# Optimization experiments

Hardware: AMD Instinct MI355X
Metric: run time of the kernel (lower is better)

## Reference

```python
import jax, jax.numpy as jnp
import numpy as np

STRIDE = (1, 1)
PAD = (1, 1)
DIL = (1, 1)
GROUPS = 1
DG = 1  # deformable_groups
KH, KW = 3, 3


def setup_inputs() -> dict:
    key = jax.random.key(0)
    k1, k2, k3, k4 = jax.random.split(key, 4)
    x = jax.random.normal(k1, (8, 256, 64, 64), jnp.float32)
    offset = jax.random.normal(k2, (8, DG * 2 * KH * KW, 64, 64), jnp.float32)
    weight = jax.random.normal(k3, (256, 256, KH, KW), jnp.float32) * 0.05
    bias = jax.random.normal(k4, (256,), jnp.float32)
    return {"x": x, "offset": offset, "weight": weight, "bias": bias}


def _deform_conv2d(x, offset, weight, bias):
    N, C, H, W = x.shape
    Cout = weight.shape[0]
    Ho = (H + 2 * PAD[0] - (DIL[0] * (KH - 1) + 1)) // STRIDE[0] + 1
    Wo = (W + 2 * PAD[1] - (DIL[1] * (KW - 1) + 1)) // STRIDE[1] + 1
    K = KH * KW
    Cg = C // DG

    # offset layout: [N, DG, K, 2(y,x), Ho, Wo]
    off = offset.reshape(N, DG, K, 2, Ho, Wo)

    ky, kx = jnp.meshgrid(jnp.arange(KH), jnp.arange(KW), indexing="ij")
    ky = (ky.reshape(K) * DIL[0]).astype(jnp.float32)  # [K]
    kx = (kx.reshape(K) * DIL[1]).astype(jnp.float32)
    base_y = (jnp.arange(Ho) * STRIDE[0] - PAD[0]).astype(jnp.float32)  # [Ho]
    base_x = (jnp.arange(Wo) * STRIDE[1] - PAD[1]).astype(jnp.float32)  # [Wo]

    # sampling positions [N, DG, K, Ho, Wo]
    py = base_y[None, None, None, :, None] + ky[None, None, :, None, None] + off[:, :, :, 0]
    px = base_x[None, None, None, None, :] + kx[None, None, :, None, None] + off[:, :, :, 1]

    y0f = jnp.floor(py)
    x0f = jnp.floor(px)
    ly = py - y0f
    lx = px - x0f
    hy = 1.0 - ly
    hx = 1.0 - lx
    y0 = y0f.astype(jnp.int32)
    x0 = x0f.astype(jnp.int32)
    y1 = y0 + 1
    x1 = x0 + 1

    img = x.reshape(N, DG, Cg, H * W)

    def gather(yi, xi):
        valid = ((yi >= 0) & (yi < H) & (xi >= 0) & (xi < W)).astype(x.dtype)
        idx = jnp.clip(yi, 0, H - 1) * W + jnp.clip(xi, 0, W - 1)  # [N,DG,K,Ho,Wo]
        flat = idx.reshape(N, DG, 1, K * Ho * Wo)
        v = jnp.take_along_axis(img, flat, axis=3).reshape(N, DG, Cg, K, Ho, Wo)
        return v * valid[:, :, None]

    # bilinear combine -> columns [N, DG, Cg, K, Ho, Wo]
    cols = (
        (hy * hx)[:, :, None] * gather(y0, x0)
        + (hy * lx)[:, :, None] * gather(y0, x1)
        + (ly * hx)[:, :, None] * gather(y1, x0)
        + (ly * lx)[:, :, None] * gather(y1, x1)
    )

    # grouped conv accumulation
    P = Ho * Wo
    cols = cols.reshape(N, GROUPS, C // GROUPS, K, P)
    w = weight.reshape(GROUPS, Cout // GROUPS, C // GROUPS, K)
    out = jnp.einsum("ngckp,gock->ngop", cols, w).reshape(N, Cout, Ho, Wo)
    return out + bias[None, :, None, None]


def reference(x, offset, weight, bias):
    return _deform_conv2d(x, offset, weight, bias)
```

## Files before the change

### kernel.cpp

```cpp
#include <hip/hip_runtime.h>


#define H 64
#define W 64
#define CIN 256
#define COUT 256
#define NIMG 8
#define KTAPS 9
#define CK (CIN * KTAPS)
#define NITER 36

typedef _Float16 f16;
typedef __attribute__((ext_vector_type(4))) _Float16 f16x4;
typedef __attribute__((ext_vector_type(8))) _Float16 f16x8;
typedef __attribute__((ext_vector_type(4))) float f32x4;

__global__ __launch_bounds__(256) void dcn_prep(const float* __restrict__ x,
                                                const float* __restrict__ w,
                                                f16* __restrict__ xt,
                                                f16* __restrict__ wt) {
    const int b = blockIdx.x;
    const int t = threadIdx.x;
    if (b < 512) {
        const int n = b >> 6, pb = b & 63;
        const int q = t & 63;
        const int hg = t >> 6;
        const float* xn = x + (size_t)n * CIN * (H * W) + pb * 64;
        float4 ld[4][4];
#pragma unroll
        for (int j = 0; j < 4; ++j)
#pragma unroll
            for (int pq = 0; pq < 4; ++pq)
                ld[j][pq] = *(const float4*)(xn + (size_t)(q * 4 + j) * (H * W) +
                                             hg * 16 + pq * 4);
        f16* xtn = xt + (size_t)n * (H * W) * CIN + (size_t)(pb * 64 + hg * 16) * CIN + q * 4;
#pragma unroll
        for (int pq = 0; pq < 4; ++pq) {
#pragma unroll
            for (int pe = 0; pe < 4; ++pe) {
                const float* l0 = (const float*)&ld[0][pq];
                const float* l1 = (const float*)&ld[1][pq];
                const float* l2 = (const float*)&ld[2][pq];
                const float* l3 = (const float*)&ld[3][pq];
                f16x4 o = {(f16)l0[pe], (f16)l1[pe], (f16)l2[pe], (f16)l3[pe]};
                *(f16x4*)(xtn + (size_t)(pq * 4 + pe) * CIN) = o;
            }
        }
    } else {
        __shared__ f16 tw[CK];
        const int co = b - 512;
        const float* wr = w + (size_t)co * CK + t * 9;
        float v[9];
#pragma unroll
        for (int j = 0; j < 9; ++j) v[j] = wr[j];
#pragma unroll
        for (int j = 0; j < 9; ++j) tw[j * 256 + t] = (f16)v[j];
        __syncthreads();
        f16* o = wt + (size_t)co * CK;
        for (int i = t; i < CK / 8; i += 256)
            *(f16x8*)(o + i * 8) = *(const f16x8*)(tw + i * 8);
    }
}

__global__ __launch_bounds__(256, 2) void dcn_mfma(
    const f16* __restrict__ xt, const float* __restrict__ offset,
    const f16* __restrict__ wt, const float* __restrict__ bias,
    float* __restrict__ out) {
    __shared__ int4 s_pix4[KTAPS][64];
    __shared__ f16 s_wbh4[KTAPS][64][4];
    __shared__ f16 s_cols[2][64][72];

    const int tid = threadIdx.x;
    const int bx = blockIdx.x;
    const int n = bx & 7;
    const int t_img = bx >> 3;
    const int tile_y = (t_img >> 3) << 3, tile_x = (t_img & 7) << 3;

    const float* offn = offset + (size_t)n * 18 * (H * W);
    for (int e = tid; e < KTAPS * 64; e += 256) {
        int k = e >> 6, p = e & 63;
        int oy = tile_y + (p >> 3), ox = tile_x + (p & 7);
        float offy = offn[(k * 2 + 0) * (H * W) + oy * W + ox];
        float offx = offn[(k * 2 + 1) * (H * W) + oy * W + ox];
        float py = (float)(oy - 1 + (k / 3)) + offy;
        float px = (float)(ox - 1 + (k % 3)) + offx;
        float y0f = floorf(py), x0f = floorf(px);
        int y0 = (int)y0f, x0 = (int)x0f, y1 = y0 + 1, x1 = x0 + 1;
        float ly = py - y0f, lx = px - x0f, hy = 1.f - ly, hx = 1.f - lx;
        bool vy0 = (y0 >= 0) && (y0 < H), vy1 = (y1 >= 0) && (y1 < H);
        bool vx0 = (x0 >= 0) && (x0 < W), vx1 = (x1 >= 0) && (x1 < W);
        int cy0 = min(max(y0, 0), H - 1), cx0 = min(max(x0, 0), W - 1);
        int cy1 = min(max(y1, 0), H - 1), cx1 = min(max(x1, 0), W - 1);
        s_pix4[k][p] = make_int4((cy0 * W + cx0) * (CIN * 2), (cy0 * W + cx1) * (CIN * 2),
                                 (cy1 * W + cx0) * (CIN * 2), (cy1 * W + cx1) * (CIN * 2));
        s_wbh4[k][p][0] = (f16)((vy0 && vx0) ? hy * hx : 0.f);
        s_wbh4[k][p][1] = (f16)((vy0 && vx1) ? hy * lx : 0.f);
        s_wbh4[k][p][2] = (f16)((vy1 && vx0) ? ly * hx : 0.f);
        s_wbh4[k][p][3] = (f16)((vy1 && vx1) ? ly * lx : 0.f);
    }

    f32x4 acc[4][4];
#pragma unroll
    for (int i = 0; i < 4; ++i)
#pragma unroll
        for (int j = 0; j < 4; ++j) acc[i][j] = (f32x4)0.f;

    const int lane = tid & 63, wv = tid >> 6;
    const int co_base = wv * 64;
    const int p_g = tid >> 2;
    const int qk = tid & 3;
    const char* xb = (const char*)(xt + (size_t)n * (H * W) * CIN);

    const f16* arow[4];
#pragma unroll
    for (int cf = 0; cf < 4; ++cf)
        arow[cf] = wt + (size_t)(co_base + 16 * cf + (lane & 15)) * CK + (lane >> 4) * 8;

    __syncthreads();

    f16x8 hb[8];
    {
        int4 cp = s_pix4[0][p_g];
        const char* b0 = xb + qk * 32;
        hb[0] = *(const f16x8*)(b0 + cp.x);
        hb[1] = *(const f16x8*)(b0 + cp.x + 16);
        hb[2] = *(const f16x8*)(b0 + cp.y);
        hb[3] = *(const f16x8*)(b0 + cp.y + 16);
        hb[4] = *(const f16x8*)(b0 + cp.z);
        hb[5] = *(const f16x8*)(b0 + cp.z + 16);
        hb[6] = *(const f16x8*)(b0 + cp.w);
        hb[7] = *(const f16x8*)(b0 + cp.w + 16);
    }

    for (int it = 0; it < NITER; ++it) {
        const int cur = it & 1;
        const int tap = it >> 2;
        {
            f16x4 wb = *(const f16x4*)&s_wbh4[tap][p_g][0];
            f16x8 v0 = hb[0] * wb[0] + hb[2] * wb[1] + hb[4] * wb[2] + hb[6] * wb[3];
            f16x8 v1 = hb[1] * wb[0] + hb[3] * wb[1] + hb[5] * wb[2] + hb[7] * wb[3];
            *(f16x8*)&s_cols[cur][p_g][qk * 16] = v0;
            *(f16x8*)&s_cols[cur][p_g][qk * 16 + 8] = v1;
        }
        if (it + 1 < NITER) {
            const int t1 = (it + 1) >> 2;
            int4 cp = s_pix4[t1][p_g];
            const char* b0 = xb + ((it + 1) & 3) * 128 + qk * 32;
            hb[0] = *(const f16x8*)(b0 + cp.x);
            hb[1] = *(const f16x8*)(b0 + cp.x + 16);
            hb[2] = *(const f16x8*)(b0 + cp.y);
            hb[3] = *(const f16x8*)(b0 + cp.y + 16);
            hb[4] = *(const f16x8*)(b0 + cp.z);
            hb[5] = *(const f16x8*)(b0 + cp.z + 16);
            hb[6] = *(const f16x8*)(b0 + cp.w);
            hb[7] = *(const f16x8*)(b0 + cp.w + 16);
        }
        f16x8 af[8];
        {
            const int k0 = it * 64;
#pragma unroll
            for (int cf = 0; cf < 4; ++cf) {
                af[cf] = *(const f16x8*)(arow[cf] + k0);
                af[4 + cf] = *(const f16x8*)(arow[cf] + k0 + 32);
            }
        }
        __syncthreads();
#pragma unroll
        for (int ks = 0; ks < 2; ++ks) {
            f16x8 bf[4];
#pragma unroll
            for (int pf = 0; pf < 4; ++pf)
                bf[pf] = *(const f16x8*)&s_cols[cur][16 * pf + (lane & 15)]
                                               [ks * 32 + (lane >> 4) * 8];
#pragma unroll
            for (int cf = 0; cf < 4; ++cf)
#pragma unroll
                for (int pf = 0; pf < 4; ++pf)
                    acc[cf][pf] = __builtin_amdgcn_mfma_f32_16x16x32_f16(
                        af[ks * 4 + cf], bf[pf], acc[cf][pf], 0, 0, 0);
        }
    }

    float* outn = out + (size_t)n * COUT * (H * W);
#pragma unroll
    for (int cf = 0; cf < 4; ++cf) {
#pragma unroll
        for (int r = 0; r < 4; ++r) {
            int co = co_base + 16 * cf + ((lane >> 4) << 2) + r;
            float b = bias[co];
#pragma unroll
            for (int pf = 0; pf < 4; ++pf) {
                int pp = 16 * pf + (lane & 15);
                int oy = tile_y + (pp >> 3), ox = tile_x + (pp & 7);
                outn[(size_t)co * (H * W) + oy * W + ox] = acc[cf][pf][r] + b;
            }
        }
    }
}

__global__ __launch_bounds__(256) void dcn_transpose_w(const float* __restrict__ w,
                                                       float* __restrict__ wt) {
    __shared__ float tile[32][33];
    const int ckb = blockIdx.x * 32;
    const int cob = blockIdx.y * 32;
    const int tx = threadIdx.x & 31;
    const int ty = threadIdx.x >> 5;
#pragma unroll
    for (int i = 0; i < 32; i += 8)
        tile[ty + i][tx] = w[(size_t)(cob + ty + i) * CK + ckb + tx];
    __syncthreads();
#pragma unroll
    for (int i = 0; i < 32; i += 8)
        wt[(size_t)(ckb + ty + i) * COUT + cob + tx] = tile[tx][ty + i];
}

__global__ __launch_bounds__(256, 2) void dcn_main(
    const float* __restrict__ x, const float* __restrict__ offset,
    const float* __restrict__ wt, const float* __restrict__ bias,
    float* __restrict__ out) {
    __shared__ int s_idx[4][KTAPS][64];
    __shared__ float s_bw[4][KTAPS][64];
    __shared__ float s_W[36][COUT];
    __shared__ float s_cols[36][64];

    const int tid = threadIdx.x;
    const int bx = blockIdx.x;
    const int n = bx >> 6;
    const int t_img = bx & 63;
    const int tile_y = (t_img >> 3) << 3;
    const int tile_x = (t_img & 7) << 3;

    const float* offn = offset + (size_t)n * 18 * (H * W);
    for (int e = tid; e < KTAPS * 64; e += 256) {
        int k = e >> 6, p = e & 63;
        int oy = tile_y + (p >> 3), ox = tile_x + (p & 7);
        float offy = offn[(k * 2 + 0) * (H * W) + oy * W + ox];
        float offx = offn[(k * 2 + 1) * (H * W) + oy * W + ox];
        float py = (float)(oy - 1 + (k / 3)) + offy;
        float px = (float)(ox - 1 + (k % 3)) + offx;
        float y0f = floorf(py), x0f = floorf(px);
        int y0 = (int)y0f, x0 = (int)x0f, y1 = y0 + 1, x1 = x0 + 1;
        float ly = py - y0f, lx = px - x0f, hy = 1.f - ly, hx = 1.f - lx;
        bool vy0 = (y0 >= 0) && (y0 < H), vy1 = (y1 >= 0) && (y1 < H);
        bool vx0 = (x0 >= 0) && (x0 < W), vx1 = (x1 >= 0) && (x1 < W);
        int cy0 = min(max(y0, 0), H - 1), cx0 = min(max(x0, 0), W - 1);
        int cy1 = min(max(y1, 0), H - 1), cx1 = min(max(x1, 0), W - 1);
        s_idx[0][k][p] = cy0 * W + cx0;
        s_idx[1][k][p] = cy0 * W + cx1;
        s_idx[2][k][p] = cy1 * W + cx0;
        s_idx[3][k][p] = cy1 * W + cx1;
        s_bw[0][k][p] = (vy0 && vx0) ? hy * hx : 0.f;
        s_bw[1][k][p] = (vy0 && vx1) ? hy * lx : 0.f;
        s_bw[2][k][p] = (vy1 && vx0) ? ly * hx : 0.f;
        s_bw[3][k][p] = (vy1 && vx1) ? ly * lx : 0.f;
    }

    float acc[8][8];
#pragma unroll
    for (int i = 0; i < 8; ++i)
#pragma unroll
        for (int j = 0; j < 8; ++j) acc[i][j] = 0.f;

    const int ty = tid >> 3;
    const int tx = tid & 7;
    const int q = tid >> 6;
    const int pl = tid & 63;
    const float* xn = x + (size_t)(n * CIN) * (H * W);

    for (int ch = 0; ch < CIN / 4; ++ch) {
        const int c0 = ch * 4;
        __syncthreads();
        {
            const int rbase = q * KTAPS;
            const int co4 = (tid & 63) * 4;
#pragma unroll
            for (int i = 0; i < KTAPS; ++i) {
                int r = rbase + i;
                *reinterpret_cast<float4*>(&s_W[r][co4]) =
                    *reinterpret_cast<const float4*>(&wt[(size_t)(c0 * KTAPS + r) * COUT + co4]);
            }
        }
#pragma unroll
        for (int s = 0; s < KTAPS; ++s) {
            int r = q + 4 * s;
            int c = r / 9;
            int k = r - c * 9;
            const float* xc = xn + (size_t)(c0 + c) * (H * W);
            float v = s_bw[0][k][pl] * xc[s_idx[0][k][pl]] +
                      s_bw[1][k][pl] * xc[s_idx[1][k][pl]] +
                      s_bw[2][k][pl] * xc[s_idx[2][k][pl]] +
                      s_bw[3][k][pl] * xc[s_idx[3][k][pl]];
            s_cols[r][pl] = v;
        }
        __syncthreads();
#pragma unroll 4
        for (int r = 0; r < 36; ++r) {
            const float4 cv0 = *reinterpret_cast<const float4*>(&s_cols[r][tx * 8]);
            const float4 cv1 = *reinterpret_cast<const float4*>(&s_cols[r][tx * 8 + 4]);
            const float4 wv0 = *reinterpret_cast<const float4*>(&s_W[r][ty * 8]);
            const float4 wv1 = *reinterpret_cast<const float4*>(&s_W[r][ty * 8 + 4]);
            const float wa[8] = {wv0.x, wv0.y, wv0.z, wv0.w, wv1.x, wv1.y, wv1.z, wv1.w};
            const float ca[8] = {cv0.x, cv0.y, cv0.z, cv0.w, cv1.x, cv1.y, cv1.z, cv1.w};
#pragma unroll
            for (int i = 0; i < 8; ++i)
#pragma unroll
                for (int j = 0; j < 8; ++j) acc[i][j] += wa[i] * ca[j];
        }
    }

    float* outn = out + (size_t)(n * COUT) * (H * W);
    const int obase = (tile_y + tx) * W + tile_x;
#pragma unroll
    for (int i = 0; i < 8; ++i) {
        int co = ty * 8 + i;
        float b = bias[co];
        float4 o0, o1;
        o0.x = acc[i][0] + b; o0.y = acc[i][1] + b; o0.z = acc[i][2] + b; o0.w = acc[i][3] + b;
        o1.x = acc[i][4] + b; o1.y = acc[i][5] + b; o1.z = acc[i][6] + b; o1.w = acc[i][7] + b;
        float* po = &outn[(size_t)co * (H * W) + obase];
        *reinterpret_cast<float4*>(po) = o0;
        *reinterpret_cast<float4*>(po + 4) = o1;
    }
}

extern "C" void kernel_launch(void* const* d_in, const int* in_sizes, int n_in,
                              void* d_out, int out_size, void* d_ws, size_t ws_size,
                              hipStream_t stream) {
    const float* x = (const float*)d_in[0];
    const float* offset = (const float*)d_in[1];
    const float* weight = (const float*)d_in[2];
    const float* bias = (const float*)d_in[3];
    float* out = (float*)d_out;

    const size_t XT_OFF = 2u * 1024 * 1024;
    const size_t need = XT_OFF + (size_t)NIMG * H * W * CIN * sizeof(f16);

    if (ws_size >= need) {
        f16* wt = (f16*)d_ws;
        f16* xt = (f16*)((char*)d_ws + XT_OFF);
        dcn_prep<<<512 + COUT, 256, 0, stream>>>(x, weight, xt, wt);
        dcn_mfma<<<NIMG * 64, 256, 0, stream>>>(xt, offset, wt, bias, out);
    } else {
        float* wtf = (float*)d_ws;
        dim3 tgrid(CK / 32, COUT / 32);
        dcn_transpose_w<<<tgrid, 256, 0, stream>>>(weight, wtf);
        dcn_main<<<NIMG * 64, 256, 0, stream>>>(x, offset, wtf, bias, out);
    }
}
```

Measured before the change: 180.5 us.

## Fuse prep and MFMA deformable conv into one cooperative kernel with grid sync

Replaces the two-kernel sequence (layout/precision prep, then MFMA deformable conv) with a single cooperative kernel. Each block first transposes its slice of x to fp16 NHWC, and blocks below COUT also convert one weight row. A grid-wide sync follows, then the same block runs the bilinear-gather plus MFMA GEMM for an 8x8 output tile. The goal is to remove one kernel launch and its tail gap. In exchange it adds a grid barrier, needs 512 co-resident blocks (launch bounds 256,2), and changes the prep access pattern to go through an LDS staging tile. It falls back to the old two-kernel path if the cooperative launch fails.

```diff
diff --git a/kernel.cpp b/kernel.cpp
--- a/kernel.cpp
+++ b/kernel.cpp
@@ -1,4 +1,7 @@
 #include <hip/hip_runtime.h>
+#include <hip/hip_cooperative_groups.h>
+
+namespace cg = cooperative_groups;
 
 
 #define H 64
@@ -14,6 +17,191 @@
 typedef __attribute__((ext_vector_type(4))) _Float16 f16x4;
 typedef __attribute__((ext_vector_type(8))) _Float16 f16x8;
 typedef __attribute__((ext_vector_type(4))) float f32x4;
+
+__global__ __launch_bounds__(256, 2) void dcn_fused(
+    const float* __restrict__ x, const float* __restrict__ offset,
+    const float* __restrict__ w, const float* __restrict__ bias,
+    f16* __restrict__ xt, f16* __restrict__ wt, float* __restrict__ out) {
+    __shared__ union SMem {
+        struct {
+            int4 pix4[KTAPS][64];
+            f16 wbh4[KTAPS][64][4];
+            f16 cols[2][64][72];
+        } m;
+        struct {
+            f16 tl[64][66];
+            f16 tw[CK];
+        } p;
+    } sm;
+
+    const int tid = threadIdx.x;
+    const int bx = blockIdx.x;
+    const int n = bx & 7;
+    const int t_img = bx >> 3;
+
+    {
+        const int pb = t_img;
+        const float* xn = x + (size_t)n * CIN * (H * W) + pb * 64;
+        f16* xtn = xt + (size_t)n * (H * W) * CIN + (size_t)(pb * 64) * CIN;
+        const int c = tid >> 4;
+        const int p4 = (tid & 15) * 4;
+        for (int cb = 0; cb < 4; ++cb) {
+#pragma unroll
+            for (int pass = 0; pass < 4; ++pass) {
+                float4 v = *(const float4*)(xn + (size_t)(cb * 64 + c + pass * 16) * (H * W) + p4);
+                const int cc = c + pass * 16;
+                sm.p.tl[p4 + 0][cc] = (f16)v.x;
+                sm.p.tl[p4 + 1][cc] = (f16)v.y;
+                sm.p.tl[p4 + 2][cc] = (f16)v.z;
+                sm.p.tl[p4 + 3][cc] = (f16)v.w;
+            }
+            __syncthreads();
+            const int p = tid >> 2, cq = (tid & 3) * 16;
+            f16* dst = xtn + (size_t)p * CIN + cb * 64 + cq;
+            *(f16x8*)dst = *(const f16x8*)&sm.p.tl[p][cq];
+            *(f16x8*)(dst + 8) = *(const f16x8*)&sm.p.tl[p][cq + 8];
+            __syncthreads();
+        }
+    }
+    if (bx < COUT) {
+        const int co = bx;
+        const float* wr = w + (size_t)co * CK + tid * 9;
+        float v[9];
+#pragma unroll
+        for (int j = 0; j < 9; ++j) v[j] = wr[j];
+#pragma unroll
+        for (int j = 0; j < 9; ++j) sm.p.tw[j * 256 + tid] = (f16)v[j];
+        __syncthreads();
+        f16* o = wt + (size_t)co * CK;
+        for (int i = tid; i < CK / 8; i += 256)
+            *(f16x8*)(o + i * 8) = *(const f16x8*)(sm.p.tw + i * 8);
+    }
+
+    cg::this_grid().sync();
+
+    const int tile_y = (t_img >> 3) << 3, tile_x = (t_img & 7) << 3;
+
+    const float* offn = offset + (size_t)n * 18 * (H * W);
+    for (int e = tid; e < KTAPS * 64; e += 256) {
+        int k = e >> 6, p = e & 63;
+        int oy = tile_y + (p >> 3), ox = tile_x + (p & 7);
+        float offy = offn[(k * 2 + 0) * (H * W) + oy * W + ox];
+        float offx = offn[(k * 2 + 1) * (H * W) + oy * W + ox];
+        float py = (float)(oy - 1 + (k / 3)) + offy;
+        float px = (float)(ox - 1 + (k % 3)) + offx;
+        float y0f = floorf(py), x0f = floorf(px);
+        int y0 = (int)y0f, x0 = (int)x0f, y1 = y0 + 1, x1 = x0 + 1;
+        float ly = py - y0f, lx = px - x0f, hy = 1.f - ly, hx = 1.f - lx;
+        bool vy0 = (y0 >= 0) && (y0 < H), vy1 = (y1 >= 0) && (y1 < H);
+        bool vx0 = (x0 >= 0) && (x0 < W), vx1 = (x1 >= 0) && (x1 < W);
+        int cy0 = min(max(y0, 0), H - 1), cx0 = min(max(x0, 0), W - 1);
+        int cy1 = min(max(y1, 0), H - 1), cx1 = min(max(x1, 0), W - 1);
+        sm.m.pix4[k][p] = make_int4((cy0 * W + cx0) * (CIN * 2), (cy0 * W + cx1) * (CIN * 2),
+                                    (cy1 * W + cx0) * (CIN * 2), (cy1 * W + cx1) * (CIN * 2));
+        sm.m.wbh4[k][p][0] = (f16)((vy0 && vx0) ? hy * hx : 0.f);
+        sm.m.wbh4[k][p][1] = (f16)((vy0 && vx1) ? hy * lx : 0.f);
+        sm.m.wbh4[k][p][2] = (f16)((vy1 && vx0) ? ly * hx : 0.f);
+        sm.m.wbh4[k][p][3] = (f16)((vy1 && vx1) ? ly * lx : 0.f);
+    }
+
+    f32x4 acc[4][4];
+#pragma unroll
+    for (int i = 0; i < 4; ++i)
+#pragma unroll
+        for (int j = 0; j < 4; ++j) acc[i][j] = (f32x4)0.f;
+
+    const int lane = tid & 63, wv = tid >> 6;
+    const int co_base = wv * 64;
+    const int p_g = tid >> 2;
+    const int qk = tid & 3;
+    const char* xb = (const char*)(xt + (size_t)n * (H * W) * CIN);
+
+    const f16* arow[4];
+#pragma unroll
+    for (int cf = 0; cf < 4; ++cf)
+        arow[cf] = wt + (size_t)(co_base + 16 * cf + (lane & 15)) * CK + (lane >> 4) * 8;
+
+    __syncthreads();
+
+    f16x8 hb[8];
+    {
+        int4 cp = sm.m.pix4[0][p_g];
+        const char* b0 = xb + qk * 32;
+        hb[0] = *(const f16x8*)(b0 + cp.x);
+        hb[1] = *(const f16x8*)(b0 + cp.x + 16);
+        hb[2] = *(const f16x8*)(b0 + cp.y);
+        hb[3] = *(const f16x8*)(b0 + cp.y + 16);
+        hb[4] = *(const f16x8*)(b0 + cp.z);
+        hb[5] = *(const f16x8*)(b0 + cp.z + 16);
+        hb[6] = *(const f16x8*)(b0 + cp.w);
+        hb[7] = *(const f16x8*)(b0 + cp.w + 16);
+    }
+
+    for (int it = 0; it < NITER; ++it) {
+        const int cur = it & 1;
+        const int tap = it >> 2;
+        {
+            f16x4 wb = *(const f16x4*)&sm.m.wbh4[tap][p_g][0];
+            f16x8 v0 = hb[0] * wb[0] + hb[2] * wb[1] + hb[4] * wb[2] + hb[6] * wb[3];
+            f16x8 v1 = hb[1] * wb[0] + hb[3] * wb[1] + hb[5] * wb[2] + hb[7] * wb[3];
+            *(f16x8*)&sm.m.cols[cur][p_g][qk * 16] = v0;
+            *(f16x8*)&sm.m.cols[cur][p_g][qk * 16 + 8] = v1;
+        }
+        if (it + 1 < NITER) {
+            const int t1 = (it + 1) >> 2;
+            int4 cp = sm.m.pix4[t1][p_g];
+            const char* b0 = xb + ((it + 1) & 3) * 128 + qk * 32;
+            hb[0] = *(const f16x8*)(b0 + cp.x);
+            hb[1] = *(const f16x8*)(b0 + cp.x + 16);
+            hb[2] = *(const f16x8*)(b0 + cp.y);
+            hb[3] = *(const f16x8*)(b0 + cp.y + 16);
+            hb[4] = *(const f16x8*)(b0 + cp.z);
+            hb[5] = *(const f16x8*)(b0 + cp.z + 16);
+            hb[6] = *(const f16x8*)(b0 + cp.w);
+            hb[7] = *(const f16x8*)(b0 + cp.w + 16);
+        }
+        f16x8 af[8];
+        {
+            const int k0 = it * 64;
+#pragma unroll
+            for (int cf = 0; cf < 4; ++cf) {
+                af[cf] = *(const f16x8*)(arow[cf] + k0);
+                af[4 + cf] = *(const f16x8*)(arow[cf] + k0 + 32);
+            }
+        }
+        __syncthreads();
+#pragma unroll
+        for (int ks = 0; ks < 2; ++ks) {
+            f16x8 bf[4];
+#pragma unroll
+            for (int pf = 0; pf < 4; ++pf)
+                bf[pf] = *(const f16x8*)&sm.m.cols[cur][16 * pf + (lane & 15)]
+                                                  [ks * 32 + (lane >> 4) * 8];
+#pragma unroll
+            for (int cf = 0; cf < 4; ++cf)
+#pragma unroll
+                for (int pf = 0; pf < 4; ++pf)
+                    acc[cf][pf] = __builtin_amdgcn_mfma_f32_16x16x32_f16(
+                        af[ks * 4 + cf], bf[pf], acc[cf][pf], 0, 0, 0);
+        }
+    }
+
+    float* outn = out + (size_t)n * COUT * (H * W);
+#pragma unroll
+    for (int cf = 0; cf < 4; ++cf) {
+#pragma unroll
+        for (int r = 0; r < 4; ++r) {
+            int co = co_base + 16 * cf + ((lane >> 4) << 2) + r;
+            float b = bias[co];
+#pragma unroll
+            for (int pf = 0; pf < 4; ++pf) {
+                int pp = 16 * pf + (lane & 15);
+                int oy = tile_y + (pp >> 3), ox = tile_x + (pp & 7);
+                outn[(size_t)co * (H * W) + oy * W + ox] = acc[cf][pf][r] + b;
+            }
+        }
+    }
+}
 
 __global__ __launch_bounds__(256) void dcn_prep(const float* __restrict__ x,
                                                 const float* __restrict__ w,
@@ -31,8 +219,7 @@
         for (int j = 0; j < 4; ++j)
 #pragma unroll
             for (int pq = 0; pq < 4; ++pq)
-                ld[j][pq] = *(const float4*)(xn + (size_t)(q * 4 + j) * (H * W) +
-                                             hg * 16 + pq * 4);
+                ld[j][pq] = *(const float4*)(xn + (size_t)(q * 4 + j) * (H * W) + hg * 16 + pq * 4);
         f16* xtn = xt + (size_t)n * (H * W) * CIN + (size_t)(pb * 64 + hg * 16) * CIN + q * 4;
 #pragma unroll
         for (int pq = 0; pq < 4; ++pq) {
@@ -338,8 +525,15 @@
     if (ws_size >= need) {
         f16* wt = (f16*)d_ws;
         f16* xt = (f16*)((char*)d_ws + XT_OFF);
-        dcn_prep<<<512 + COUT, 256, 0, stream>>>(x, weight, xt, wt);
-        dcn_mfma<<<NIMG * 64, 256, 0, stream>>>(xt, offset, wt, bias, out);
+
+        void* args[] = {(void*)&x, (void*)&offset, (void*)&weight, (void*)&bias,
+                        (void*)&xt, (void*)&wt, (void*)&out};
+        hipError_t err = hipLaunchCooperativeKernel((const void*)dcn_fused, dim3(512),
+                                                    dim3(256), args, 0, stream);
+        if (err != hipSuccess) {
+            dcn_prep<<<512 + COUT, 256, 0, stream>>>(x, weight, xt, wt);
+            dcn_mfma<<<NIMG * 64, 256, 0, stream>>>(xt, offset, wt, bias, out);
+        }
     } else {
         float* wtf = (float*)d_ws;
         dim3 tgrid(CK / 32, COUT / 32);
```

Result: slower. 262.8 us (+45.6%).
